# Kernel optimization log

Hardware: AMD Instinct MI355X
Metric: run time of the kernel (lower is better)

Reference implementation:

```python
import jax, jax.numpy as jnp
import numpy as np

NUM_CLASSES = 80
TOPK = 10            # matcher_hpy['topk_candicate']
ALPHA = 0.25         # focal_loss_alpha
GAMMA = 2.0          # focal_loss_gamma
REG_COST_W = 3.0     # SimOTA iou-cost weight
INVALID_COST = 1e9

B, SIDE, STRIDE, G = 16, 160, 8, 32
M = SIDE * SIDE
IMG = SIDE * STRIDE


def _bce_logits(x, t):
    # stable binary_cross_entropy_with_logits
    return t * jax.nn.softplus(-x) + (1.0 - t) * jax.nn.softplus(x)


def _box_iou_pairwise(b1, b2, eps=1e-8):
    # b1: [G,4], b2: [M,4] (xyxy) -> [G,M]
    tl = jnp.maximum(b1[:, None, :2], b2[None, :, :2])
    br = jnp.minimum(b1[:, None, 2:], b2[None, :, 2:])
    wh = jnp.clip(br - tl, 0.0)
    inter = wh[..., 0] * wh[..., 1]
    a1 = (b1[:, 2] - b1[:, 0]) * (b1[:, 3] - b1[:, 1])
    a2 = (b2[:, 2] - b2[:, 0]) * (b2[:, 3] - b2[:, 1])
    union = a1[:, None] + a2[None, :] - inter
    return inter / jnp.maximum(union, eps)


def _giou(b1, b2, eps=1e-7):
    # elementwise GIoU, b1/b2: [N,4] xyxy -> [N]
    tl = jnp.maximum(b1[..., :2], b2[..., :2])
    br = jnp.minimum(b1[..., 2:], b2[..., 2:])
    wh = jnp.clip(br - tl, 0.0)
    inter = wh[..., 0] * wh[..., 1]
    a1 = jnp.clip(b1[..., 2] - b1[..., 0], 0.0) * jnp.clip(b1[..., 3] - b1[..., 1], 0.0)
    a2 = jnp.clip(b2[..., 2] - b2[..., 0], 0.0) * jnp.clip(b2[..., 3] - b2[..., 1], 0.0)
    union = a1 + a2 - inter
    iou = inter / jnp.maximum(union, eps)
    ctl = jnp.minimum(b1[..., :2], b2[..., :2])
    cbr = jnp.maximum(b1[..., 2:], b2[..., 2:])
    cwh = jnp.clip(cbr - ctl, 0.0)
    carea = jnp.maximum(cwh[..., 0] * cwh[..., 1], eps)
    return iou - (carea - union) / carea


def _simota(anchors, pred_cls, pred_box, gt_labels, gt_boxes):
    # per-image AlignedSimOTA (mmyolo DSL-style dynamic-k assignment)
    # anchors [M,2], pred_cls [M,C] (logits, detached), pred_box [M,4], gt_labels [G], gt_boxes [G,4]
    num_gt = gt_boxes.shape[0]
    num_anchor = anchors.shape[0]
    # anchor point strictly inside gt box: [G, M]
    deltas = jnp.concatenate([anchors[None, :, :] - gt_boxes[:, None, :2],
                              gt_boxes[:, None, 2:] - anchors[None, :, :]], axis=-1)
    is_in_gt = deltas.min(axis=-1) > 0.0
    valid_anchor = is_in_gt.any(axis=0)                      # [M]
    ious = _box_iou_pairwise(gt_boxes, pred_box)             # [G, M]
    reg_cost = -jnp.log(ious + 1e-8)
    # aligned classification cost: logit at gt class, soft target = IoU
    logits = pred_cls[:, gt_labels].T                        # [G, M]
    scale = jnp.abs(ious - jax.nn.sigmoid(logits)) ** 2.0
    cls_cost = _bce_logits(logits, ious) * scale
    cost = cls_cost + REG_COST_W * reg_cost                  # [G, M]
    cost = jnp.where(valid_anchor[None, :], cost, INVALID_COST)
    # dynamic k: sum of topk ious per gt, int, clamped min 1 (<= TOPK)
    topk_ious = jax.lax.top_k(ious, TOPK)[0]                 # [G, TOPK]
    dyn_k = jnp.clip(topk_ious.sum(axis=-1).astype(jnp.int32), 1, None)  # [G]
    # lowest-cost TOPK candidates per gt, keep rank < dyn_k
    _, cand_idx = jax.lax.top_k(-cost, TOPK)                 # [G, TOPK]
    sel = (jnp.arange(TOPK)[None, :] < dyn_k[:, None]).astype(jnp.float32)
    matching = jnp.zeros((num_gt, num_anchor), jnp.float32).at[
        jnp.arange(num_gt)[:, None], cand_idx].add(sel)      # [G, M]
    fg = matching.sum(axis=0) > 0                            # [M]
    # conflicts (anchor matched to >1 gt) resolved by min cost
    matched_gt = jnp.argmin(jnp.where(matching > 0, cost, jnp.inf), axis=0)  # [M]
    labels = jnp.where(fg, gt_labels[matched_gt], NUM_CLASSES)
    boxes = jnp.where(fg[:, None], gt_boxes[matched_gt], 0.0)
    return labels, boxes


def _rand_boxes(key, shape):
    k1, k2 = jax.random.split(key)
    ctr = jax.random.uniform(k1, shape + (2,), minval=0.0, maxval=float(IMG))
    wh = jax.random.uniform(k2, shape + (2,), minval=16.0, maxval=256.0)
    return jnp.clip(jnp.concatenate([ctr - wh * 0.5, ctr + wh * 0.5], axis=-1), 0.0, float(IMG))


def setup_inputs() -> dict:
    key = jax.random.key(0)
    k0, k1, k2, k3 = jax.random.split(key, 4)
    pred_cls = jax.random.normal(k0, (B, M, NUM_CLASSES), jnp.float32) - 4.0  # background-biased logits
    pred_box = _rand_boxes(k1, (B, M))
    gt_boxes = _rand_boxes(k2, (B, G))
    gt_labels = jax.random.randint(k3, (B, G), 0, NUM_CLASSES, dtype=jnp.int32)
    ys, xs = jnp.meshgrid(jnp.arange(SIDE), jnp.arange(SIDE), indexing='ij')
    anchors = (jnp.stack([xs, ys], axis=-1).reshape(-1, 2).astype(jnp.float32) + 0.5) * STRIDE
    mask = jnp.zeros((B, M), dtype=bool)  # outputs['mask']: True = padded position
    return {"pred_cls": pred_cls, "pred_box": pred_box, "anchors": anchors,
            "gt_boxes": gt_boxes, "gt_labels": gt_labels, "mask": mask}


def reference(pred_cls, pred_box, anchors, gt_boxes, gt_labels, mask):
    C = pred_cls.shape[-1]
    # matcher consumes detached predictions
    lbl, btgt = jax.vmap(_simota, in_axes=(None, 0, 0, 0, 0))(
        anchors,
        jax.lax.stop_gradient(pred_cls),
        jax.lax.stop_gradient(pred_box),
        gt_labels, gt_boxes)
    cls_t = lbl.reshape(-1)                                   # [B*M]
    pos = cls_t != C                                          # (cls_t >= 0) always holds
    num_fgs = jnp.maximum(pos.sum().astype(jnp.float32), 1.0)
    valid = jnp.logical_not(mask.reshape(-1))                 # mask & (cls_t >= 0)
    # sigmoid focal loss over all valid anchors, one-hot targets (class C -> all-zero row)
    x = pred_cls.reshape(-1, C)
    t = jax.nn.one_hot(cls_t, C, dtype=x.dtype)
    p = jax.nn.sigmoid(x)
    ce = _bce_logits(x, t)
    p_t = p * t + (1.0 - p) * (1.0 - t)
    focal = ce * (1.0 - p_t) ** GAMMA * (ALPHA * t + (1.0 - ALPHA) * (1.0 - t))
    loss_cls = (focal * valid[:, None].astype(x.dtype)).sum() / num_fgs
    # GIoU loss over positives
    g = _giou(pred_box.reshape(-1, 4), btgt.reshape(-1, 4))
    loss_giou = ((1.0 - g) * pos.astype(x.dtype)).sum() / num_fgs
    return jnp.stack([loss_cls, loss_giou])
```

## Files before the change

### kernel.cpp

```cpp
#include <hip/hip_runtime.h>
#include <cstdint>
#include <cstddef>

#define NB 16
#define SIDE 160
#define MM (SIDE*SIDE)
#define NC 80
#define NG 32
#define TOPK 10
#define REGW 3.0f
#define INVC 1e9f

using ull = unsigned long long;

__device__ __forceinline__ unsigned f2sort(float f) {
    unsigned b = __float_as_uint(f);
    return b ^ ((unsigned)((int)b >> 31) | 0x80000000u);
}
__device__ __forceinline__ float rcpf(float x) { return __builtin_amdgcn_rcpf(x); }

__device__ __forceinline__ float f_bg(float x) {
    float e  = __expf(-fabsf(x));
    float rc = rcpf(1.f + e);
    float p  = (x >= 0.f) ? rc : e*rc;
    float sp = fmaxf(x, 0.f) + __logf(1.f + e);
    return sp*p*p*0.75f;
}
__device__ __forceinline__ float f_fg(float x) {
    float e  = __expf(-fabsf(x));
    float rc = rcpf(1.f + e);
    float p  = (x >= 0.f) ? rc : e*rc;
    float sp = fmaxf(x, 0.f) + __logf(1.f + e);
    float om = 1.f - p;
    return (sp - x)*om*om*0.25f;
}

__global__ __launch_bounds__(256) void k_valid(const float* __restrict__ anchors,
                                               const float* __restrict__ gt_boxes,
                                               unsigned char* __restrict__ valid) {
    int i = blockIdx.x * 256 + threadIdx.x;
    int b = i / MM, m = i % MM;
    float ax = anchors[2*m], ay = anchors[2*m+1];
    const float* gb = gt_boxes + b*NG*4;
    unsigned char v = 0;
    for (int g = 0; g < NG; ++g) {
        float x1 = gb[4*g], y1 = gb[4*g+1], x2 = gb[4*g+2], y2 = gb[4*g+3];
        float d = fminf(fminf(ax-x1, ay-y1), fminf(x2-ax, y2-ay));
        v |= (d > 0.f) ? 1 : 0;
    }
    valid[i] = v;
}

__global__ __launch_bounds__(512, 4) void k_cost(
    const float* __restrict__ pred_cls, const float* __restrict__ pred_box,
    const float* __restrict__ gt_boxes, const int* __restrict__ gt_labels,
    const unsigned char* __restrict__ valid, const unsigned char* __restrict__ mask,
    unsigned* __restrict__ cost_part, unsigned* __restrict__ iou_part,
    float* __restrict__ accum, int nchunk)
{
    __shared__ float s_cls[64*33];
    __shared__ float4 s_box[64];
    __shared__ unsigned char s_vld[64];
    __shared__ float s_gtb[128];
    __shared__ int s_lab[32];
    __shared__ int s_slot[80];
    __shared__ float s_red[8];

    int blk = blockIdx.x;
    int b = blk / nchunk, chunk = blk - b*nchunk;
    int A = MM / nchunk;
    int nsub = A >> 6;
    int tid = threadIdx.x;
    int g = tid >> 4, j = tid & 15;

    if (tid < 128) s_gtb[tid] = gt_boxes[b*NG*4 + tid];
    if (tid < 32)  s_lab[tid] = gt_labels[b*NG + tid];
    if (tid < 80)  s_slot[tid] = 9999;
    __syncthreads();
    if (tid < 32) atomicMin(&s_slot[s_lab[tid]], tid);
    __syncthreads();

    float gx1 = s_gtb[g*4+0], gy1 = s_gtb[g*4+1];
    float gx2 = s_gtb[g*4+2], gy2 = s_gtb[g*4+3];
    int slot = s_slot[s_lab[g]];
    float garea = (gx2-gx1)*(gy2-gy1);

    unsigned lc[TOPK], li[TOPK];
    #pragma unroll
    for (int t = 0; t < TOPK; ++t) { lc[t] = 0xFFFFFFFFu; li[t] = 0xFFFFFFFFu; }
    float bgsum = 0.f;

    int m0 = chunk * A;
    for (int s = 0; s < nsub; ++s) {
        int mbase = m0 + s*64;
        size_t gbase = (size_t)b*MM + mbase;
        __syncthreads();
        if (tid < 64) {
            s_box[tid] = ((const float4*)pred_box)[gbase + tid];
            s_vld[tid] = valid[gbase + tid];
        }
        const float4* gcls = (const float4*)(pred_cls + gbase*NC);
        #pragma unroll
        for (int q = 0; q < 3; ++q) {
            int idx = tid + 512*q;
            if (idx < 1280) {
                float4 v = gcls[idx];
                int a = idx / 20, c0 = (idx - a*20)*4;
                int t0 = s_slot[c0], t1 = s_slot[c0+1], t2 = s_slot[c0+2], t3 = s_slot[c0+3];
                if (t0 < 64) s_cls[a*33 + t0] = v.x;
                if (t1 < 64) s_cls[a*33 + t1] = v.y;
                if (t2 < 64) s_cls[a*33 + t2] = v.z;
                if (t3 < 64) s_cls[a*33 + t3] = v.w;
                if (!mask[gbase + a])
                    bgsum += f_bg(v.x) + f_bg(v.y) + f_bg(v.z) + f_bg(v.w);
            }
        }
        __syncthreads();
        #pragma unroll
        for (int k = 0; k < 4; ++k) {
            int a = j + 16*k;
            unsigned m = (unsigned)(mbase + a);
            float4 pb = s_box[a];
            float iw = fmaxf(fminf(gx2, pb.z) - fmaxf(gx1, pb.x), 0.f);
            float ih = fmaxf(fminf(gy2, pb.w) - fmaxf(gy1, pb.y), 0.f);
            float inter = iw*ih;
            float pa = (pb.z-pb.x)*(pb.w-pb.y);
            float uni = garea + pa - inter;
            float iou = inter * rcpf(fmaxf(uni, 1e-8f));
            float l = s_cls[a*33 + slot];
            float e  = __expf(-fabsf(l));
            float rc = rcpf(1.f + e);
            float sg = (l >= 0.f) ? rc : e*rc;
            float sp_pos = fmaxf(l, 0.f) + __logf(1.f + e);
            float sp_neg = sp_pos - l;
            float bce = iou*sp_neg + (1.f-iou)*sp_pos;
            float dd = iou - sg;
            float cost = bce*dd*dd - REGW*__logf(iou + 1e-8f);
            if (!s_vld[a]) cost = INVC;
            unsigned cur = (f2sort(cost) & 0xFFFF8000u) | m;
            #pragma unroll
            for (int t = 0; t < TOPK; ++t) {
                unsigned mn = min(lc[t], cur), mx = max(lc[t], cur);
                lc[t] = mn; cur = mx;
            }
            cur = (~f2sort(iou) & 0xFFFF8000u) | m;
            #pragma unroll
            for (int t = 0; t < TOPK; ++t) {
                unsigned mn = min(li[t], cur), mx = max(li[t], cur);
                li[t] = mn; cur = mx;
            }
        }
    }
    size_t pbase = ((size_t)(b*NG + g)*nchunk + chunk)*TOPK;
    #pragma unroll
    for (int r = 0; r < TOPK; ++r) {
        unsigned h = lc[0];
        h = min(h, (unsigned)__shfl_xor((int)h, 1));
        h = min(h, (unsigned)__shfl_xor((int)h, 2));
        h = min(h, (unsigned)__shfl_xor((int)h, 4));
        h = min(h, (unsigned)__shfl_xor((int)h, 8));
        if (lc[0] == h) {
            #pragma unroll
            for (int t = 0; t < TOPK-1; ++t) lc[t] = lc[t+1];
            lc[TOPK-1] = 0xFFFFFFFFu;
        }
        if (j == 0) cost_part[pbase + r] = h;
    }
    #pragma unroll
    for (int r = 0; r < TOPK; ++r) {
        unsigned h = li[0];
        h = min(h, (unsigned)__shfl_xor((int)h, 1));
        h = min(h, (unsigned)__shfl_xor((int)h, 2));
        h = min(h, (unsigned)__shfl_xor((int)h, 4));
        h = min(h, (unsigned)__shfl_xor((int)h, 8));
        if (li[0] == h) {
            #pragma unroll
            for (int t = 0; t < TOPK-1; ++t) li[t] = li[t+1];
            li[TOPK-1] = 0xFFFFFFFFu;
        }
        if (j == 0) iou_part[pbase + r] = h;
    }
    for (int o = 32; o; o >>= 1) bgsum += __shfl_down(bgsum, o);
    int ln = tid & 63, wv = tid >> 6;
    if (ln == 0) s_red[wv] = bgsum;
    __syncthreads();
    if (tid == 0) {
        float sum = 0.f;
        #pragma unroll
        for (int w = 0; w < 8; ++w) sum += s_red[w];
        atomicAdd(&accum[0], sum);
    }
}

__global__ __launch_bounds__(256) void k_merge(
    const unsigned* __restrict__ cost_part, const unsigned* __restrict__ iou_part,
    const float* __restrict__ pred_cls, const float* __restrict__ pred_box,
    const float* __restrict__ gt_boxes, const int* __restrict__ gt_labels,
    const unsigned char* __restrict__ valid,
    ull* __restrict__ best, int nchunk)
{
    int lane = threadIdx.x & 63, wv = threadIdx.x >> 6;
    int bg = blockIdx.x*4 + wv;
    int b = bg >> 5, g = bg & (NG-1);
    int nent = nchunk * TOPK;
    size_t base = (size_t)bg * nent;

    float gx1 = gt_boxes[bg*4+0], gy1 = gt_boxes[bg*4+1];
    float gx2 = gt_boxes[bg*4+2], gy2 = gt_boxes[bg*4+3];
    int   lab = gt_labels[bg];
    float garea = (gx2-gx1)*(gy2-gy1);

    unsigned l10[TOPK];
    #pragma unroll
    for (int t = 0; t < TOPK; ++t) l10[t] = 0xFFFFFFFFu;
    for (int q = 0; q*64 < nent; ++q) {
        int e = lane + 64*q;
        unsigned cur = (e < nent) ? iou_part[base + e] : 0xFFFFFFFFu;
        #pragma unroll
        for (int t = 0; t < TOPK; ++t) {
            unsigned mn = min(l10[t], cur), mx = max(l10[t], cur);
            l10[t] = mn; cur = mx;
        }
    }
    unsigned ioukey = 0xFFFFFFFFu;
    #pragma unroll
    for (int r = 0; r < TOPK; ++r) {
        unsigned h = l10[0];
        #pragma unroll
        for (int mlt = 1; mlt < 64; mlt <<= 1)
            h = min(h, (unsigned)__shfl_xor((int)h, mlt));
        if (l10[0] == h) {
            #pragma unroll
            for (int t = 0; t < TOPK-1; ++t) l10[t] = l10[t+1];
            l10[TOPK-1] = 0xFFFFFFFFu;
        }
        if (lane == r) ioukey = h;
    }
    float myiou = 0.f;
    if (lane < TOPK) {
        int m = (int)(ioukey & 0x7FFFu);
        float4 pb = ((const float4*)pred_box)[(size_t)b*MM + m];
        float iw = fmaxf(fminf(gx2, pb.z) - fmaxf(gx1, pb.x), 0.f);
        float ih = fmaxf(fminf(gy2, pb.w) - fmaxf(gy1, pb.y), 0.f);
        float inter = iw*ih;
        float pa = (pb.z-pb.x)*(pb.w-pb.y);
        float uni = garea + pa - inter;
        myiou = inter / fmaxf(uni, 1e-8f);
    }
    #pragma unroll
    for (int mlt = 1; mlt < 64; mlt <<= 1) myiou += __shfl_xor(myiou, mlt);
    int dynk = (int)myiou; if (dynk < 1) dynk = 1;

    #pragma unroll
    for (int t = 0; t < TOPK; ++t) l10[t] = 0xFFFFFFFFu;
    for (int q = 0; q*64 < nent; ++q) {
        int e = lane + 64*q;
        unsigned cur = (e < nent) ? cost_part[base + e] : 0xFFFFFFFFu;
        #pragma unroll
        for (int t = 0; t < TOPK; ++t) {
            unsigned mn = min(l10[t], cur), mx = max(l10[t], cur);
            l10[t] = mn; cur = mx;
        }
    }
    unsigned costkey = 0xFFFFFFFFu;
    #pragma unroll
    for (int r = 0; r < TOPK; ++r) {
        unsigned h = l10[0];
        #pragma unroll
        for (int mlt = 1; mlt < 64; mlt <<= 1)
            h = min(h, (unsigned)__shfl_xor((int)h, mlt));
        if (l10[0] == h) {
            #pragma unroll
            for (int t = 0; t < TOPK-1; ++t) l10[t] = l10[t+1];
            l10[TOPK-1] = 0xFFFFFFFFu;
        }
        if (lane == r) costkey = h;
    }
    if (lane < dynk) {
        unsigned m = costkey & 0x7FFFu;
        size_t gi = (size_t)b*MM + m;
        float cost;
        if (!valid[gi]) {
            cost = INVC;
        } else {
            float4 pb = ((const float4*)pred_box)[gi];
            float iw = fmaxf(fminf(gx2, pb.z) - fmaxf(gx1, pb.x), 0.f);
            float ih = fmaxf(fminf(gy2, pb.w) - fmaxf(gy1, pb.y), 0.f);
            float inter = iw*ih;
            float pa = (pb.z-pb.x)*(pb.w-pb.y);
            float uni = garea + pa - inter;
            float iou = inter / fmaxf(uni, 1e-8f);
            float l = pred_cls[gi*NC + lab];
            float e  = expf(-fabsf(l));
            float p  = 1.f/(1.f + e);
            float sg = (l >= 0.f) ? p : e*p;
            float sp_pos = fmaxf(l, 0.f) + log1pf(e);
            float sp_neg = sp_pos - l;
            float bce = iou*sp_neg + (1.f-iou)*sp_pos;
            float dd = iou - sg;
            cost = bce*dd*dd - REGW*logf(iou + 1e-8f);
        }
        atomicMin(&best[(size_t)b*MM + m], ((ull)f2sort(cost) << 32) | (unsigned)g);
    }
}

__global__ __launch_bounds__(256) void k_post(
    const float* __restrict__ pred_cls, const float* __restrict__ pred_box,
    const float* __restrict__ gt_boxes, const int* __restrict__ gt_labels,
    const unsigned char* __restrict__ mask, const ull* __restrict__ best,
    float* __restrict__ accum)
{
    int i = blockIdx.x*256 + threadIdx.x;
    int b = i / MM;
    ull key = best[i];
    float cls_c = 0.f, giou_c = 0.f, cnt = 0.f;
    if (key != ~0ull) {
        int g = (int)(key & 0xFFFFFFFFull);
        int bgi = b*NG + g;
        float4 pb = *(const float4*)(pred_box + (size_t)i*4);
        float gx1 = gt_boxes[bgi*4],   gy1 = gt_boxes[bgi*4+1];
        float gx2 = gt_boxes[bgi*4+2], gy2 = gt_boxes[bgi*4+3];
        float iw = fmaxf(fminf(pb.z,gx2) - fmaxf(pb.x,gx1), 0.f);
        float ih = fmaxf(fminf(pb.w,gy2) - fmaxf(pb.y,gy1), 0.f);
        float inter = iw*ih;
        float a1 = fmaxf(pb.z-pb.x,0.f)*fmaxf(pb.w-pb.y,0.f);
        float a2 = fmaxf(gx2-gx1,0.f)*fmaxf(gy2-gy1,0.f);
        float uni = a1 + a2 - inter;
        float iou = inter / fmaxf(uni, 1e-7f);
        float cw = fmaxf(fmaxf(pb.z,gx2) - fminf(pb.x,gx1), 0.f);
        float ch = fmaxf(fmaxf(pb.w,gy2) - fminf(pb.y,gy1), 0.f);
        float ca = fmaxf(cw*ch, 1e-7f);
        float giou = iou - (ca - uni)/ca;
        giou_c = 1.f - giou;
        cnt = 1.f;
        if (!mask[i]) {
            int lab = gt_labels[bgi];
            float x = pred_cls[(size_t)i*NC + lab];
            cls_c = f_fg(x) - f_bg(x);
        }
    }
    for (int o = 32; o; o >>= 1) {
        cls_c  += __shfl_down(cls_c, o);
        giou_c += __shfl_down(giou_c, o);
        cnt    += __shfl_down(cnt, o);
    }
    __shared__ float sc[4], sg_[4], sn[4];
    int ln = threadIdx.x & 63, wv = threadIdx.x >> 6;
    if (ln == 0) { sc[wv] = cls_c; sg_[wv] = giou_c; sn[wv] = cnt; }
    __syncthreads();
    if (threadIdx.x == 0) {
        atomicAdd(&accum[0], sc[0]+sc[1]+sc[2]+sc[3]);
        float gtot = sg_[0]+sg_[1]+sg_[2]+sg_[3];
        float ntot = sn[0]+sn[1]+sn[2]+sn[3];
        if (gtot != 0.f || ntot != 0.f) {
            atomicAdd(&accum[1], gtot);
            atomicAdd(&accum[2], ntot);
        }
    }
}

__global__ void k_final(const float* __restrict__ accum, float* __restrict__ out) {
    if (threadIdx.x == 0) {
        float nf = fmaxf(accum[2], 1.f);
        out[0] = accum[0]/nf;
        out[1] = accum[1]/nf;
    }
}

extern "C" void kernel_launch(void* const* d_in, const int* in_sizes, int n_in,
                              void* d_out, int out_size, void* d_ws, size_t ws_size,
                              hipStream_t stream) {
    const float* pred_cls  = (const float*)d_in[0];
    const float* pred_box  = (const float*)d_in[1];
    const float* anchors   = (const float*)d_in[2];
    const float* gt_boxes  = (const float*)d_in[3];
    const int*   gt_labels = (const int*)d_in[4];
    const unsigned char* mask = (const unsigned char*)d_in[5];
    float* out = (float*)d_out;

    auto need = [](int nc) -> size_t {
        return 256 + (size_t)NB*MM*8 + (size_t)NB*MM + 2*(size_t)NB*NG*nc*TOPK*4;
    };
    int nchunk = 50;
    if (ws_size < need(50)) nchunk = 25;
    if (ws_size < need(25)) return;

    char* ws = (char*)d_ws;
    float* accum = (float*)ws;
    ull* best = (ull*)(ws + 256);
    unsigned char* valid = (unsigned char*)(ws + 256 + (size_t)NB*MM*8);
    unsigned* cost_part = (unsigned*)(ws + 256 + (size_t)NB*MM*8 + (size_t)NB*MM);
    unsigned* iou_part  = cost_part + (size_t)NB*NG*nchunk*TOPK;

    hipMemsetAsync(accum, 0, 16, stream);
    hipMemsetAsync(best, 0xFF, (size_t)NB*MM*8, stream);

    k_valid<<<NB*MM/256, 256, 0, stream>>>(anchors, gt_boxes, valid);
    k_cost <<<NB*nchunk, 512, 0, stream>>>(pred_cls, pred_box, gt_boxes, gt_labels,
                                           valid, mask, cost_part, iou_part, accum, nchunk);
    k_merge<<<NB*NG/4,   256, 0, stream>>>(cost_part, iou_part, pred_cls, pred_box,
                                           gt_boxes, gt_labels, valid, best, nchunk);
    k_post <<<NB*MM/256, 256, 0, stream>>>(pred_cls, pred_box, gt_boxes, gt_labels,
                                           mask, best, accum);
    k_final<<<1, 64, 0, stream>>>(accum, out);
}
```

Baseline: 179.2 us.

## Drop LDS staging in cost kernel, read class logits and boxes directly

Removes the shared-memory staging of per-GT class logits, pred boxes and valid flags, along with the per-subtile barriers. Each thread now loads its box, its GT-label logit and its valid byte straight from global memory and relies on cache hits after the bulk coalesced class-row read. The launch bound is raised to 8 blocks per CU, and the anchor range is split into more chunks (80) for more parallelism. The trade is scattered uncoalesced global reads and larger partial top-k buffers for k_merge to scan, in exchange for fewer syncs and less LDS.

```diff
diff --git a/kernel.cpp b/kernel.cpp
--- a/kernel.cpp
+++ b/kernel.cpp
@@ -51,19 +51,15 @@
     valid[i] = v;
 }
 
-__global__ __launch_bounds__(512, 4) void k_cost(
+__global__ __launch_bounds__(512, 8) void k_cost(
     const float* __restrict__ pred_cls, const float* __restrict__ pred_box,
     const float* __restrict__ gt_boxes, const int* __restrict__ gt_labels,
     const unsigned char* __restrict__ valid, const unsigned char* __restrict__ mask,
     unsigned* __restrict__ cost_part, unsigned* __restrict__ iou_part,
     float* __restrict__ accum, int nchunk)
 {
-    __shared__ float s_cls[64*33];
-    __shared__ float4 s_box[64];
-    __shared__ unsigned char s_vld[64];
     __shared__ float s_gtb[128];
     __shared__ int s_lab[32];
-    __shared__ int s_slot[80];
     __shared__ float s_red[8];
 
     int blk = blockIdx.x;
@@ -75,14 +71,11 @@
 
     if (tid < 128) s_gtb[tid] = gt_boxes[b*NG*4 + tid];
     if (tid < 32)  s_lab[tid] = gt_labels[b*NG + tid];
-    if (tid < 80)  s_slot[tid] = 9999;
-    __syncthreads();
-    if (tid < 32) atomicMin(&s_slot[s_lab[tid]], tid);
     __syncthreads();
 
     float gx1 = s_gtb[g*4+0], gy1 = s_gtb[g*4+1];
     float gx2 = s_gtb[g*4+2], gy2 = s_gtb[g*4+3];
-    int slot = s_slot[s_lab[g]];
+    int   lab = s_lab[g];
     float garea = (gx2-gx1)*(gy2-gy1);
 
     unsigned lc[TOPK], li[TOPK];
@@ -94,40 +87,31 @@
     for (int s = 0; s < nsub; ++s) {
         int mbase = m0 + s*64;
         size_t gbase = (size_t)b*MM + mbase;
-        __syncthreads();
-        if (tid < 64) {
-            s_box[tid] = ((const float4*)pred_box)[gbase + tid];
-            s_vld[tid] = valid[gbase + tid];
-        }
         const float4* gcls = (const float4*)(pred_cls + gbase*NC);
         #pragma unroll
         for (int q = 0; q < 3; ++q) {
             int idx = tid + 512*q;
             if (idx < 1280) {
                 float4 v = gcls[idx];
-                int a = idx / 20, c0 = (idx - a*20)*4;
-                int t0 = s_slot[c0], t1 = s_slot[c0+1], t2 = s_slot[c0+2], t3 = s_slot[c0+3];
-                if (t0 < 64) s_cls[a*33 + t0] = v.x;
-                if (t1 < 64) s_cls[a*33 + t1] = v.y;
-                if (t2 < 64) s_cls[a*33 + t2] = v.z;
-                if (t3 < 64) s_cls[a*33 + t3] = v.w;
+                int a = idx / 20;
                 if (!mask[gbase + a])
                     bgsum += f_bg(v.x) + f_bg(v.y) + f_bg(v.z) + f_bg(v.w);
             }
         }
-        __syncthreads();
         #pragma unroll
         for (int k = 0; k < 4; ++k) {
             int a = j + 16*k;
             unsigned m = (unsigned)(mbase + a);
-            float4 pb = s_box[a];
+            size_t gi = gbase + a;
+            float4 pb = ((const float4*)pred_box)[gi];
+            float l  = pred_cls[gi*NC + lab];
+            unsigned char vld = valid[gi];
             float iw = fmaxf(fminf(gx2, pb.z) - fmaxf(gx1, pb.x), 0.f);
             float ih = fmaxf(fminf(gy2, pb.w) - fmaxf(gy1, pb.y), 0.f);
             float inter = iw*ih;
             float pa = (pb.z-pb.x)*(pb.w-pb.y);
             float uni = garea + pa - inter;
             float iou = inter * rcpf(fmaxf(uni, 1e-8f));
-            float l = s_cls[a*33 + slot];
             float e  = __expf(-fabsf(l));
             float rc = rcpf(1.f + e);
             float sg = (l >= 0.f) ? rc : e*rc;
@@ -136,7 +120,7 @@
             float bce = iou*sp_neg + (1.f-iou)*sp_pos;
             float dd = iou - sg;
             float cost = bce*dd*dd - REGW*__logf(iou + 1e-8f);
-            if (!s_vld[a]) cost = INVC;
+            if (!vld) cost = INVC;
             unsigned cur = (f2sort(cost) & 0xFFFF8000u) | m;
             #pragma unroll
             for (int t = 0; t < TOPK; ++t) {
@@ -381,8 +365,9 @@
     auto need = [](int nc) -> size_t {
         return 256 + (size_t)NB*MM*8 + (size_t)NB*MM + 2*(size_t)NB*NG*nc*TOPK*4;
     };
-    int nchunk = 50;
-    if (ws_size < need(50)) nchunk = 25;
+    int nchunk = 80;
+    if (ws_size < need(80)) nchunk = 40;
+    if (ws_size < need(40)) nchunk = 25;
     if (ws_size < need(25)) return;
 
     char* ws = (char*)d_ws;
```

Result: faster. 169.1 us (-5.6%).
